# Kernel tuning notes

Hardware: AMD Instinct MI355X
Metric: run time of the kernel (lower is better)

The kernel has to match this reference:

```python
import jax, jax.numpy as jnp
import numpy as np

B, S, D, F, E, DT, K = 4, 2048, 1024, 4096, 8, 256, 2


def setup_inputs() -> dict:
    key = jax.random.key(0)
    ks = jax.random.split(key, 8)
    scale_g = 1.0 / np.sqrt(D)
    scale_t = 1.0 / np.sqrt(DT)
    scale_1 = 1.0 / np.sqrt(D)
    scale_2 = 1.0 / np.sqrt(F)
    return {
        "inputs": jax.random.normal(ks[0], (B, S, D), dtype=jnp.float32),
        "task_param": jax.random.normal(ks[1], (B, 1, DT), dtype=jnp.float32),
        "Wg_in": jax.random.normal(ks[2], (D, E), dtype=jnp.float32) * scale_g,
        "bg_in": jnp.zeros((E,), dtype=jnp.float32),
        "Wg_task": jax.random.normal(ks[3], (DT, E), dtype=jnp.float32) * scale_t,
        "bg_task": jnp.zeros((E,), dtype=jnp.float32),
        "alpha": jnp.float32(0.5),
        "W1": jax.random.normal(ks[4], (E, D, F), dtype=jnp.float32) * scale_1,
        "b1": jnp.zeros((E, F), dtype=jnp.float32),
        "W2": jax.random.normal(ks[5], (E, F, D), dtype=jnp.float32) * scale_2,
        "b2": jnp.zeros((E, D), dtype=jnp.float32),
    }


def reference(inputs, task_param, Wg_in, bg_in, Wg_task, bg_task, alpha, W1, b1, W2, b2):
    # Gating: blend input-gate and task-gate logits ([B,1,E] broadcasts over S)
    input_logits = jnp.einsum('bsd,de->bse', inputs, Wg_in) + bg_in
    task_logits = jnp.einsum('btd,de->bte', task_param, Wg_task) + bg_task
    gate_logits = (1.0 - alpha) * input_logits + alpha * task_logits  # [B,S,E]

    topk_vals, selected = jax.lax.top_k(gate_logits, K)  # [B,S,K]

    # Load-balancing auxiliary loss (float32 softmax, as in the original)
    weights_softmax = jax.nn.softmax(gate_logits.astype(jnp.float32), axis=-1).astype(inputs.dtype)
    average_weight = jnp.mean(weights_softmax, axis=(0, 1))  # [E]
    onehot = jax.nn.one_hot(selected, E, dtype=inputs.dtype)  # [B,S,K,E]
    average_count = jnp.mean(onehot.sum(axis=2), axis=(0, 1))  # [E]
    l_aux = jnp.mean(average_weight * average_count) * E

    # Combine weights: softmax over the top-k gate values
    w = jax.nn.softmax(topk_vals.astype(jnp.float32), axis=-1).astype(inputs.dtype)  # [B,S,K]

    # Dense expert compute (same math as the per-expert gather/scatter loop)
    h = jax.nn.silu(jnp.einsum('bsd,edf->ebsf', inputs, W1) + b1[:, None, None, :])  # [E,B,S,F]
    expert_out = jnp.einsum('ebsf,efd->ebsd', h, W2) + b2[:, None, None, :]          # [E,B,S,D]

    picked = jnp.einsum('bske,ebsd->bskd', onehot, expert_out)  # [B,S,K,D]
    results = jnp.einsum('bsk,bskd->bsd', w, picked)            # [B,S,D]
    return results, l_aux.astype(jnp.float32)
```

## Files before the change

kernel.cpp:

```cpp
#include <hip/hip_runtime.h>

#define T_TOK 8192
#define D_DIM 1024
#define F_DIM 4096
#define E_EXP 8
#define DT_DIM 256
#define GBLK 256

#define A_XB   0u
#define A_WT   16777216u
#define A_H    83886080u
#define A_Y    226492416u
#define A_META 262144000u
#define MO_FILL   0
#define MO_PB     64
#define MO_NT     128
#define MO_PARTP  256
#define MO_PARTC  8448
#define MO_TILEE  16640
#define MO_TILERB 17664
#define MO_ROUTEE 18688
#define MO_ROUTEW 84224
#define MO_TSLOT  149760
#define MO_PTOK   215296
#define META_BYTES 284928
#define META_INTS  (META_BYTES/4)

using bf16x8 = __attribute__((ext_vector_type(8))) short;
using f32x4  = __attribute__((ext_vector_type(4))) float;
typedef unsigned short u16;

__device__ __forceinline__ u16 f2bf(float f) {
  union { float f; unsigned u; } v; v.f = f;
  unsigned r = v.u + 0x7FFFu + ((v.u >> 16) & 1u);
  return (u16)(r >> 16);
}
__device__ __forceinline__ float bf2f(u16 h) {
  union { unsigned u; float f; } v; v.u = ((unsigned)h) << 16; return v.f;
}
__device__ __forceinline__ void gload16(const void* gsrc, void* ldst) {
  __builtin_amdgcn_global_load_lds(
      (const __attribute__((address_space(1))) void*)gsrc,
      (__attribute__((address_space(3))) void*)ldst, 16, 0, 0);
}

__global__ void zerok(int* p, int n) {
  int i = blockIdx.x * 256 + threadIdx.x;
  if (i < n) p[i] = 0;
}

__global__ __launch_bounds__(256) void tcvt(const float* __restrict__ src,
                                            u16* __restrict__ dst, int R, int C) {
  __shared__ u16 tile[32][33];
  size_t off = (size_t)blockIdx.z * R * C;
  int cb = blockIdx.x * 32, rb = blockIdx.y * 32;
  int tx = threadIdx.x & 31, ty = threadIdx.x >> 5;
#pragma unroll
  for (int i = 0; i < 4; i++)
    tile[ty + i * 8][tx] = f2bf(src[off + (size_t)(rb + ty + i * 8) * C + cb + tx]);
  __syncthreads();
#pragma unroll
  for (int i = 0; i < 4; i++)
    dst[off + (size_t)(cb + ty + i * 8) * R + rb + tx] = tile[tx][ty + i * 8];
}

__global__ __launch_bounds__(256) void gating(
    const float* __restrict__ X, const float* __restrict__ TP,
    const float* __restrict__ Wg, const float* __restrict__ bg,
    const float* __restrict__ Wt, const float* __restrict__ bgt,
    const float* __restrict__ alphaP, u16* __restrict__ Xb, int* meta) {
  __shared__ float WgT[E_EXP * D_DIM];
  __shared__ float WtT[E_EXP * DT_DIM];
  __shared__ float wsP[4][8];
  __shared__ int   wsC[4][8];
  int tid = threadIdx.x;
  for (int i = tid; i < E_EXP * D_DIM; i += 256) { int d = i >> 3, e = i & 7; WgT[e * D_DIM + d] = Wg[i]; }
  for (int i = tid; i < E_EXP * DT_DIM; i += 256) { int d = i >> 3, e = i & 7; WtT[e * DT_DIM + d] = Wt[i]; }
  __syncthreads();
  int lane = tid & 63, wid = tid >> 6;
  int tb = blockIdx.x * 32;
  int b = tb >> 11;
  float alpha = alphaP[0];

  float tac[8] = {};
#pragma unroll
  for (int i = 0; i < 4; i++) {
    int d = lane + i * 64;
    float x = TP[b * DT_DIM + d];
#pragma unroll
    for (int e = 0; e < 8; e++) tac[e] += x * WtT[e * DT_DIM + d];
  }
  for (int off = 32; off > 0; off >>= 1)
#pragma unroll
    for (int e = 0; e < 8; e++) tac[e] += __shfl_xor(tac[e], off);
  float tl[8];
#pragma unroll
  for (int e = 0; e < 8; e++) tl[e] = alpha * (tac[e] + bgt[e]);

  float psum[8] = {};
  int   cnt[8] = {};
  for (int i = 0; i < 8; i++) {
    int t = tb + wid * 8 + i;
    const float* xr = X + (size_t)t * D_DIM;
    float acc[8] = {};
    u16 xb[16];
#pragma unroll 4
    for (int j = 0; j < 16; j++) {
      int d = lane + j * 64;
      float x = xr[d];
      xb[j] = f2bf(x);
#pragma unroll
      for (int e = 0; e < 8; e++) acc[e] += x * WgT[e * D_DIM + d];
    }
#pragma unroll
    for (int j = 0; j < 16; j++) Xb[(size_t)t * D_DIM + lane + j * 64] = xb[j];
    for (int off = 32; off > 0; off >>= 1)
#pragma unroll
      for (int e = 0; e < 8; e++) acc[e] += __shfl_xor(acc[e], off);
    float gl[8];
#pragma unroll
    for (int e = 0; e < 8; e++) gl[e] = (1.f - alpha) * (acc[e] + bg[e]) + tl[e];
    int e1 = 0;
#pragma unroll
    for (int e = 1; e < 8; e++) if (gl[e] > gl[e1]) e1 = e;
    int es = (e1 == 0) ? 1 : 0;
#pragma unroll
    for (int e = 0; e < 8; e++) if (e != e1 && gl[e] > gl[es]) es = e;
    float mx = gl[0];
#pragma unroll
    for (int e = 1; e < 8; e++) mx = fmaxf(mx, gl[e]);
    float pe[8], se = 0.f;
#pragma unroll
    for (int e = 0; e < 8; e++) { pe[e] = __expf(gl[e] - mx); se += pe[e]; }
    float inv = 1.f / se;
    if (lane == 0) {
#pragma unroll
      for (int e = 0; e < 8; e++) psum[e] += pe[e] * inv;
      cnt[e1]++; cnt[es]++;
      float w1 = 1.f / (1.f + __expf(gl[es] - gl[e1]));
      meta[MO_ROUTEE / 4 + 2 * t] = e1;
      meta[MO_ROUTEE / 4 + 2 * t + 1] = es;
      ((float*)meta)[MO_ROUTEW / 4 + 2 * t] = w1;
      ((float*)meta)[MO_ROUTEW / 4 + 2 * t + 1] = 1.f - w1;
    }
  }
  if (lane == 0) {
#pragma unroll
    for (int e = 0; e < 8; e++) { wsP[wid][e] = psum[e]; wsC[wid][e] = cnt[e]; }
  }
  __syncthreads();
  if (tid < 8) {
    float p = wsP[0][tid] + wsP[1][tid] + wsP[2][tid] + wsP[3][tid];
    int   c = wsC[0][tid] + wsC[1][tid] + wsC[2][tid] + wsC[3][tid];
    ((float*)meta)[MO_PARTP / 4 + blockIdx.x * 8 + tid] = p;
    meta[MO_PARTC / 4 + blockIdx.x * 8 + tid] = c;
  }
}

__global__ void plan(int* meta, float* out) {
  __shared__ float sp[8];
  __shared__ int   sc[8];
  int tid = threadIdx.x;
  if (blockIdx.x != 0) return;
  if (tid < 8) {
    const float* pp = (const float*)meta + MO_PARTP / 4;
    const int*   pc = meta + MO_PARTC / 4;
    float p = 0.f; int c = 0;
    for (int b = 0; b < GBLK; b++) { p += pp[b * 8 + tid]; c += pc[b * 8 + tid]; }
    sp[tid] = p; sc[tid] = c;
  }
  __syncthreads();
  if (tid == 0) {
    int* pb = meta + MO_PB / 4;
    int* tileE = meta + MO_TILEE / 4;
    int* tileRB = meta + MO_TILERB / 4;
    int base = 0, nt = 0;
    float la = 0.f;
    for (int e = 0; e < 8; e++) {
      int n = sc[e];
      pb[e] = base;
      int ntl = (n + 127) >> 7;
      for (int i = 0; i < ntl; i++) { tileE[nt] = e; tileRB[nt] = base + (i << 7); nt++; }
      base += ntl << 7;
      la += (sp[e] * (1.f / 8192.f)) * ((float)n * (1.f / 8192.f));
    }
    pb[8] = base;
    meta[MO_NT / 4] = nt;
    out[T_TOK * D_DIM] = la;
  }
}

__global__ __launch_bounds__(256) void fillk(int* meta) {
  int t = blockIdx.x * 256 + threadIdx.x;
  int lane = threadIdx.x & 63;
  int* pb = meta + MO_PB / 4;
  int* fl = meta + MO_FILL / 4;
  int* ptok = meta + MO_PTOK / 4;
  int* ts = meta + MO_TSLOT / 4;
  unsigned long long lmask = (lane == 63) ? ~0ull >> 1 : ((1ull << (lane + 1)) - 1) >> 1;
  lmask = (1ull << lane) - 1;
#pragma unroll
  for (int k = 0; k < 2; k++) {
    int e = meta[MO_ROUTEE / 4 + 2 * t + k];
    int slot = 0;
    for (int ee = 0; ee < 8; ee++) {
      unsigned long long mask = __ballot(e == ee);
      if (e == ee) {
        int low = __ffsll((long long)mask) - 1;
        int pre = __popcll(mask & lmask);
        int base = 0;
        if (lane == low) base = atomicAdd(&fl[ee], __popcll(mask));
        base = __shfl(base, low);
        slot = pb[ee] + base + pre;
      }
    }
    ptok[slot] = t;
    ts[2 * t + k] = slot;
  }
}

__global__ __launch_bounds__(256) void gemm1(
    const u16* __restrict__ Xb, const u16* __restrict__ W1T,
    const float* __restrict__ b1, u16* __restrict__ H, const int* __restrict__ meta) {
  int nt = meta[MO_NT / 4];
  int bt = blockIdx.x;
  if (bt >= nt) return;
  int e = meta[MO_TILEE / 4 + bt];
  int rb = meta[MO_TILERB / 4 + bt];
  int cb = blockIdx.y * 128;
  const int* ptok = meta + MO_PTOK / 4;

  __shared__ short sA[128 * 32];
  __shared__ short sB[128 * 32];
  int tid = threadIdx.x, lane = tid & 63, wid = tid >> 6;
  int wr = wid >> 1, wc = wid & 1;
  int r0 = tid >> 2, c0 = (tid & 3) << 3;
  int tok0 = ptok[rb + r0];
  int tok1 = ptok[rb + r0 + 64];
  const u16* gA0 = Xb + (size_t)tok0 * D_DIM + c0;
  const u16* gA1 = Xb + (size_t)tok1 * D_DIM + c0;
  const u16* gB0 = W1T + ((size_t)e * F_DIM + cb + r0) * D_DIM + c0;
  const u16* gB1 = gB0 + (size_t)64 * D_DIM;
  char* lA = (char*)sA + wid * 1024;
  char* lB = (char*)sB + wid * 1024;

  f32x4 acc[4][4] = {};
  for (int k0 = 0; k0 < D_DIM; k0 += 32) {
    __syncthreads();
    gload16(gA0 + k0, lA);
    gload16(gA1 + k0, lA + 4096);
    gload16(gB0 + k0, lB);
    gload16(gB1 + k0, lB + 4096);
    __syncthreads();
    bf16x8 af[4], bfr[4];
    int ra = wr * 64 + (lane & 15), kb = (lane >> 4) << 3;
#pragma unroll
    for (int m = 0; m < 4; m++)
      af[m] = *(const bf16x8*)((const char*)sA + ((ra + m * 16) * 32 + kb) * 2);
    int rn = wc * 64 + (lane & 15);
#pragma unroll
    for (int n = 0; n < 4; n++)
      bfr[n] = *(const bf16x8*)((const char*)sB + ((rn + n * 16) * 32 + kb) * 2);
#pragma unroll
    for (int m = 0; m < 4; m++)
#pragma unroll
      for (int n = 0; n < 4; n++)
        acc[m][n] = __builtin_amdgcn_mfma_f32_16x16x32_bf16(af[m], bfr[n], acc[m][n], 0, 0, 0);
  }
  int rbase = wr * 64 + ((lane >> 4) << 2);
  int cbase = cb + wc * 64 + (lane & 15);
#pragma unroll
  for (int m = 0; m < 4; m++)
#pragma unroll
    for (int n = 0; n < 4; n++) {
      int f = cbase + n * 16;
      float bias = b1[e * F_DIM + f];
#pragma unroll
      for (int r = 0; r < 4; r++) {
        int p = rb + rbase + m * 16 + r;
        float v = acc[m][n][r] + bias;
        float s = v * (1.0f / (1.0f + __expf(-v)));
        H[(size_t)p * F_DIM + f] = f2bf(s);
      }
    }
}

__global__ __launch_bounds__(256) void gemm2(
    const u16* __restrict__ H, const u16* __restrict__ W2T,
    const float* __restrict__ b2, u16* __restrict__ Y, const int* __restrict__ meta) {
  int nt = meta[MO_NT / 4];
  int bt = blockIdx.x;
  if (bt >= nt) return;
  int e = meta[MO_TILEE / 4 + bt];
  int rb = meta[MO_TILERB / 4 + bt];
  int cb = blockIdx.y * 128;
  __shared__ short sA[128 * 32];
  __shared__ short sB[128 * 32];
  int tid = threadIdx.x, lane = tid & 63, wid = tid >> 6;
  int wr = wid >> 1, wc = wid & 1;
  int r0 = tid >> 2, c0 = (tid & 3) << 3;
  const u16* gA0 = H + (size_t)(rb + r0) * F_DIM + c0;
  const u16* gA1 = gA0 + (size_t)64 * F_DIM;
  const u16* gB0 = W2T + ((size_t)e * D_DIM + cb + r0) * F_DIM + c0;
  const u16* gB1 = gB0 + (size_t)64 * F_DIM;
  char* lA = (char*)sA + wid * 1024;
  char* lB = (char*)sB + wid * 1024;

  f32x4 acc[4][4] = {};
  for (int k0 = 0; k0 < F_DIM; k0 += 32) {
    __syncthreads();
    gload16(gA0 + k0, lA);
    gload16(gA1 + k0, lA + 4096);
    gload16(gB0 + k0, lB);
    gload16(gB1 + k0, lB + 4096);
    __syncthreads();
    bf16x8 af[4], bfr[4];
    int ra = wr * 64 + (lane & 15), kb = (lane >> 4) << 3;
#pragma unroll
    for (int m = 0; m < 4; m++)
      af[m] = *(const bf16x8*)((const char*)sA + ((ra + m * 16) * 32 + kb) * 2);
    int rn = wc * 64 + (lane & 15);
#pragma unroll
    for (int n = 0; n < 4; n++)
      bfr[n] = *(const bf16x8*)((const char*)sB + ((rn + n * 16) * 32 + kb) * 2);
#pragma unroll
    for (int m = 0; m < 4; m++)
#pragma unroll
      for (int n = 0; n < 4; n++)
        acc[m][n] = __builtin_amdgcn_mfma_f32_16x16x32_bf16(af[m], bfr[n], acc[m][n], 0, 0, 0);
  }
  int rbase = wr * 64 + ((lane >> 4) << 2);
  int cbase = cb + wc * 64 + (lane & 15);
#pragma unroll
  for (int m = 0; m < 4; m++)
#pragma unroll
    for (int n = 0; n < 4; n++) {
      int d = cbase + n * 16;
      float bias = b2[e * D_DIM + d];
#pragma unroll
      for (int r = 0; r < 4; r++) {
        int p = rb + rbase + m * 16 + r;
        Y[(size_t)p * D_DIM + d] = f2bf(acc[m][n][r] + bias);
      }
    }
}

__global__ __launch_bounds__(256) void combine(const u16* __restrict__ Y,
                                               const int* __restrict__ meta,
                                               float* __restrict__ out) {
  int t = blockIdx.x;
  const int* ts = meta + MO_TSLOT / 4;
  const float* rw = (const float*)meta + MO_ROUTEW / 4;
  int s1 = ts[2 * t], s2 = ts[2 * t + 1];
  float w1 = rw[2 * t], w2 = rw[2 * t + 1];
  int d0 = threadIdx.x * 4;
  ushort4 a = *(const ushort4*)(Y + (size_t)s1 * D_DIM + d0);
  ushort4 b = *(const ushort4*)(Y + (size_t)s2 * D_DIM + d0);
  float4 v;
  v.x = w1 * bf2f(a.x) + w2 * bf2f(b.x);
  v.y = w1 * bf2f(a.y) + w2 * bf2f(b.y);
  v.z = w1 * bf2f(a.z) + w2 * bf2f(b.z);
  v.w = w1 * bf2f(a.w) + w2 * bf2f(b.w);
  *(float4*)(out + (size_t)t * D_DIM + d0) = v;
}

extern "C" void kernel_launch(void* const* d_in, const int* in_sizes, int n_in,
                              void* d_out, int out_size, void* d_ws, size_t ws_size,
                              hipStream_t stream) {
  (void)in_sizes; (void)n_in; (void)out_size; (void)ws_size;
  const float* X    = (const float*)d_in[0];
  const float* TP   = (const float*)d_in[1];
  const float* Wg   = (const float*)d_in[2];
  const float* bg   = (const float*)d_in[3];
  const float* Wt   = (const float*)d_in[4];
  const float* bgt  = (const float*)d_in[5];
  const float* alp  = (const float*)d_in[6];
  const float* W1   = (const float*)d_in[7];
  const float* b1   = (const float*)d_in[8];
  const float* W2   = (const float*)d_in[9];
  const float* b2   = (const float*)d_in[10];
  float* out = (float*)d_out;
  char* ws = (char*)d_ws;
  u16* Xb = (u16*)(ws + A_XB);
  u16* WT = (u16*)(ws + A_WT);
  u16* H  = (u16*)(ws + A_H);
  u16* Y  = (u16*)(ws + A_Y);
  int* meta = (int*)(ws + A_META);

  zerok<<<(META_INTS + 255) / 256, 256, 0, stream>>>(meta, META_INTS);
  tcvt<<<dim3(F_DIM / 32, D_DIM / 32, E_EXP), 256, 0, stream>>>(W1, WT, D_DIM, F_DIM);
  gating<<<GBLK, 256, 0, stream>>>(X, TP, Wg, bg, Wt, bgt, alp, Xb, meta);
  plan<<<1, 64, 0, stream>>>(meta, out);
  fillk<<<T_TOK / 256, 256, 0, stream>>>(meta);
  gemm1<<<dim3(136, F_DIM / 128), 256, 0, stream>>>(Xb, WT, b1, H, meta);
  tcvt<<<dim3(D_DIM / 32, F_DIM / 32, E_EXP), 256, 0, stream>>>(W2, WT, F_DIM, D_DIM);
  gemm2<<<dim3(136, D_DIM / 128), 256, 0, stream>>>(H, WT, b2, Y, meta);
  combine<<<T_TOK, 256, 0, stream>>>(Y, meta, out);
}
```

Before: 636.8 us.

## Double K-tile depth to 64 with XOR-swizzled LDS and reorder gemm2 grid

```diff
diff --git a/kernel.cpp b/kernel.cpp
--- a/kernel.cpp
+++ b/kernel.cpp
@@ -197,8 +197,7 @@
   int* fl = meta + MO_FILL / 4;
   int* ptok = meta + MO_PTOK / 4;
   int* ts = meta + MO_TSLOT / 4;
-  unsigned long long lmask = (lane == 63) ? ~0ull >> 1 : ((1ull << (lane + 1)) - 1) >> 1;
-  lmask = (1ull << lane) - 1;
+  unsigned long long lmask = (1ull << lane) - 1;
 #pragma unroll
   for (int k = 0; k < 2; k++) {
     int e = meta[MO_ROUTEE / 4 + 2 * t + k];
@@ -219,6 +218,7 @@
   }
 }
 
+
 __global__ __launch_bounds__(256) void gemm1(
     const u16* __restrict__ Xb, const u16* __restrict__ W1T,
     const float* __restrict__ b1, u16* __restrict__ H, const int* __restrict__ meta) {
@@ -230,42 +230,50 @@
   int cb = blockIdx.y * 128;
   const int* ptok = meta + MO_PTOK / 4;
 
-  __shared__ short sA[128 * 32];
-  __shared__ short sB[128 * 32];
+  __shared__ short sA[128 * 64];
+  __shared__ short sB[128 * 64];
   int tid = threadIdx.x, lane = tid & 63, wid = tid >> 6;
   int wr = wid >> 1, wc = wid & 1;
-  int r0 = tid >> 2, c0 = (tid & 3) << 3;
-  int tok0 = ptok[rb + r0];
-  int tok1 = ptok[rb + r0 + 64];
-  const u16* gA0 = Xb + (size_t)tok0 * D_DIM + c0;
-  const u16* gA1 = Xb + (size_t)tok1 * D_DIM + c0;
-  const u16* gB0 = W1T + ((size_t)e * F_DIM + cb + r0) * D_DIM + c0;
-  const u16* gB1 = gB0 + (size_t)64 * D_DIM;
-  char* lA = (char*)sA + wid * 1024;
-  char* lB = (char*)sB + wid * 1024;
+
+  int gsrc = ((lane & 7) ^ (lane >> 3)) * 8;
+  const u16* srcA[4];
+  const u16* srcB[4];
+#pragma unroll
+  for (int c = 0; c < 4; c++) {
+    int rr = c * 32 + wid * 8 + (lane >> 3);
+    int tok = ptok[rb + rr];
+    srcA[c] = Xb + (size_t)tok * D_DIM + gsrc;
+    srcB[c] = W1T + ((size_t)e * F_DIM + cb + rr) * D_DIM + gsrc;
+  }
 
   f32x4 acc[4][4] = {};
-  for (int k0 = 0; k0 < D_DIM; k0 += 32) {
+  int g0 = lane >> 4, swz = lane & 7;
+  int ra = wr * 64 + (lane & 15);
+  int rn = wc * 64 + (lane & 15);
+  for (int k0 = 0; k0 < D_DIM; k0 += 64) {
     __syncthreads();
-    gload16(gA0 + k0, lA);
-    gload16(gA1 + k0, lA + 4096);
-    gload16(gB0 + k0, lB);
-    gload16(gB1 + k0, lB + 4096);
+#pragma unroll
+    for (int c = 0; c < 4; c++) {
+      gload16(srcA[c] + k0, (char*)sA + c * 4096 + wid * 1024);
+      gload16(srcB[c] + k0, (char*)sB + c * 4096 + wid * 1024);
+    }
     __syncthreads();
-    bf16x8 af[4], bfr[4];
-    int ra = wr * 64 + (lane & 15), kb = (lane >> 4) << 3;
-#pragma unroll
-    for (int m = 0; m < 4; m++)
-      af[m] = *(const bf16x8*)((const char*)sA + ((ra + m * 16) * 32 + kb) * 2);
-    int rn = wc * 64 + (lane & 15);
-#pragma unroll
-    for (int n = 0; n < 4; n++)
-      bfr[n] = *(const bf16x8*)((const char*)sB + ((rn + n * 16) * 32 + kb) * 2);
-#pragma unroll
-    for (int m = 0; m < 4; m++)
+#pragma unroll
+    for (int kk = 0; kk < 2; kk++) {
+      bf16x8 af[4], bf[4];
+      int gg = ((kk * 4 + g0) ^ swz) * 8;
+#pragma unroll
+      for (int m = 0; m < 4; m++)
+        af[m] = *(const bf16x8*)(sA + (ra + m * 16) * 64 + gg);
 #pragma unroll
       for (int n = 0; n < 4; n++)
-        acc[m][n] = __builtin_amdgcn_mfma_f32_16x16x32_bf16(af[m], bfr[n], acc[m][n], 0, 0, 0);
+        bf[n] = *(const bf16x8*)(sB + (rn + n * 16) * 64 + gg);
+#pragma unroll
+      for (int m = 0; m < 4; m++)
+#pragma unroll
+        for (int n = 0; n < 4; n++)
+          acc[m][n] = __builtin_amdgcn_mfma_f32_16x16x32_bf16(af[m], bf[n], acc[m][n], 0, 0, 0);
+    }
   }
   int rbase = wr * 64 + ((lane >> 4) << 2);
   int cbase = cb + wc * 64 + (lane & 15);
@@ -289,45 +297,55 @@
     const u16* __restrict__ H, const u16* __restrict__ W2T,
     const float* __restrict__ b2, u16* __restrict__ Y, const int* __restrict__ meta) {
   int nt = meta[MO_NT / 4];
-  int bt = blockIdx.x;
+  int bt = blockIdx.y;
   if (bt >= nt) return;
   int e = meta[MO_TILEE / 4 + bt];
   int rb = meta[MO_TILERB / 4 + bt];
-  int cb = blockIdx.y * 128;
-  __shared__ short sA[128 * 32];
-  __shared__ short sB[128 * 32];
+  int cb = blockIdx.x * 128;
+
+  __shared__ short sA[128 * 64];
+  __shared__ short sB[128 * 64];
   int tid = threadIdx.x, lane = tid & 63, wid = tid >> 6;
   int wr = wid >> 1, wc = wid & 1;
-  int r0 = tid >> 2, c0 = (tid & 3) << 3;
-  const u16* gA0 = H + (size_t)(rb + r0) * F_DIM + c0;
-  const u16* gA1 = gA0 + (size_t)64 * F_DIM;
-  const u16* gB0 = W2T + ((size_t)e * D_DIM + cb + r0) * F_DIM + c0;
-  const u16* gB1 = gB0 + (size_t)64 * F_DIM;
-  char* lA = (char*)sA + wid * 1024;
-  char* lB = (char*)sB + wid * 1024;
+
+  int gsrc = ((lane & 7) ^ (lane >> 3)) * 8;
+  const u16* srcA[4];
+  const u16* srcB[4];
+#pragma unroll
+  for (int c = 0; c < 4; c++) {
+    int rr = c * 32 + wid * 8 + (lane >> 3);
+    srcA[c] = H + (size_t)(rb + rr) * F_DIM + gsrc;
+    srcB[c] = W2T + ((size_t)e * D_DIM + cb + rr) * F_DIM + gsrc;
+  }
 
   f32x4 acc[4][4] = {};
-  for (int k0 = 0; k0 < F_DIM; k0 += 32) {
+  int g0 = lane >> 4, swz = lane & 7;
+  int ra = wr * 64 + (lane & 15);
+  int rn = wc * 64 + (lane & 15);
+  for (int k0 = 0; k0 < F_DIM; k0 += 64) {
     __syncthreads();
-    gload16(gA0 + k0, lA);
-    gload16(gA1 + k0, lA + 4096);
-    gload16(gB0 + k0, lB);
-    gload16(gB1 + k0, lB + 4096);
+#pragma unroll
+    for (int c = 0; c < 4; c++) {
+      gload16(srcA[c] + k0, (char*)sA + c * 4096 + wid * 1024);
+      gload16(srcB[c] + k0, (char*)sB + c * 4096 + wid * 1024);
+    }
     __syncthreads();
-    bf16x8 af[4], bfr[4];
-    int ra = wr * 64 + (lane & 15), kb = (lane >> 4) << 3;
-#pragma unroll
-    for (int m = 0; m < 4; m++)
-      af[m] = *(const bf16x8*)((const char*)sA + ((ra + m * 16) * 32 + kb) * 2);
-    int rn = wc * 64 + (lane & 15);
-#pragma unroll
-    for (int n = 0; n < 4; n++)
-      bfr[n] = *(const bf16x8*)((const char*)sB + ((rn + n * 16) * 32 + kb) * 2);
-#pragma unroll
-    for (int m = 0; m < 4; m++)
+#pragma unroll
+    for (int kk = 0; kk < 2; kk++) {
+      bf16x8 af[4], bf[4];
+      int gg = ((kk * 4 + g0) ^ swz) * 8;
+#pragma unroll
+      for (int m = 0; m < 4; m++)
+        af[m] = *(const bf16x8*)(sA + (ra + m * 16) * 64 + gg);
 #pragma unroll
       for (int n = 0; n < 4; n++)
-        acc[m][n] = __builtin_amdgcn_mfma_f32_16x16x32_bf16(af[m], bfr[n], acc[m][n], 0, 0, 0);
+        bf[n] = *(const bf16x8*)(sB + (rn + n * 16) * 64 + gg);
+#pragma unroll
+      for (int m = 0; m < 4; m++)
+#pragma unroll
+        for (int n = 0; n < 4; n++)
+          acc[m][n] = __builtin_amdgcn_mfma_f32_16x16x32_bf16(af[m], bf[n], acc[m][n], 0, 0, 0);
+    }
   }
   int rbase = wr * 64 + ((lane >> 4) << 2);
   int cbase = cb + wc * 64 + (lane & 15);
@@ -394,6 +412,6 @@
   fillk<<<T_TOK / 256, 256, 0, stream>>>(meta);
   gemm1<<<dim3(136, F_DIM / 128), 256, 0, stream>>>(Xb, WT, b1, H, meta);
   tcvt<<<dim3(D_DIM / 32, F_DIM / 32, E_EXP), 256, 0, stream>>>(W2, WT, F_DIM, D_DIM);
-  gemm2<<<dim3(136, D_DIM / 128), 256, 0, stream>>>(H, WT, b2, Y, meta);
+  gemm2<<<dim3(8, 136), 256, 0, stream>>>(H, WT, b2, Y, meta);
   combine<<<T_TOK, 256, 0, stream>>>(Y, meta, out);
 }
```

Result: slower. 660.3 us (+3.7%).
